# Performance work log

Measured on AMD Instinct MI355X. Metric: run time of the kernel, lower is better.

Reference implementation:

```python
import jax, jax.numpy as jnp
import numpy as np

N = 50000      # nodes
E = 800000     # edges
IN_DIM = 128
HID = 16       # per-head hidden dim (layer1)
HEADS = 8
OUT_DIM = 32   # layer2 output dim (1 head)
NEG_SLOPE = 0.2  # GAT-paper LeakyReLU slope


def _gat_layer(x, W, a_src, a_dst, src, dst, num_nodes):
    """One multi-head GAT layer.
    x: [N, Fin]; W: [Fin, H*D]; a_src/a_dst: [H, D]; src/dst: [E].
    Returns [N, H, D].
    """
    H, D = a_src.shape
    z = (x @ W).reshape(num_nodes, H, D)            # [N, H, D]
    # edge attention logits: attn_fc([z_src || z_dst]) split into two dots
    e_s = jnp.einsum('nhd,hd->nh', z, a_src)        # [N, H]
    e_d = jnp.einsum('nhd,hd->nh', z, a_dst)        # [N, H]
    e = e_s[src] + e_d[dst]                          # [E, H]
    e = jnp.where(e >= 0, e, NEG_SLOPE * e)          # leaky_relu
    # softmax over incoming edges of each destination node
    m = jax.ops.segment_max(e, dst, num_segments=num_nodes)   # [N, H]
    ex = jnp.exp(e - m[dst])                                   # [E, H]
    s = jax.ops.segment_sum(ex, dst, num_segments=num_nodes)  # [N, H]
    alpha = ex / s[dst]                                        # [E, H]
    msg = alpha[:, :, None] * z[src]                            # [E, H, D]
    return jax.ops.segment_sum(msg, dst, num_segments=num_nodes)  # [N, H, D]


def setup_inputs() -> dict:
    key = jax.random.key(0)
    ks = jax.random.split(key, 9)
    h = jax.random.normal(ks[0], (N, IN_DIM), dtype=jnp.float32)
    src = jax.random.randint(ks[1], (E,), 0, N, dtype=jnp.int32)
    dst = jax.random.randint(ks[2], (E,), 0, N, dtype=jnp.int32)
    sc1 = 1.0 / np.sqrt(IN_DIM)
    W1 = jax.random.normal(ks[3], (IN_DIM, HEADS * HID), dtype=jnp.float32) * sc1
    a1_src = jax.random.normal(ks[4], (HEADS, HID), dtype=jnp.float32) * 0.1
    a1_dst = jax.random.normal(ks[5], (HEADS, HID), dtype=jnp.float32) * 0.1
    sc2 = 1.0 / np.sqrt(HEADS * HID)
    W2 = jax.random.normal(ks[6], (HEADS * HID, OUT_DIM), dtype=jnp.float32) * sc2
    a2_src = jax.random.normal(ks[7], (1, OUT_DIM), dtype=jnp.float32) * 0.1
    a2_dst = jax.random.normal(ks[8], (1, OUT_DIM), dtype=jnp.float32) * 0.1
    return {"h": h, "W1": W1, "a1_src": a1_src, "a1_dst": a1_dst,
            "W2": W2, "a2_src": a2_src, "a2_dst": a2_dst,
            "src": src, "dst": dst}


def reference(h, W1, a1_src, a1_dst, W2, a2_src, a2_dst, src, dst):
    # layer1: multi-head, concat heads -> [N, HEADS*HID]
    h1 = _gat_layer(h, W1, a1_src, a1_dst, src, dst, N).reshape(N, HEADS * HID)
    h1 = jax.nn.elu(h1)
    # layer2: single head -> [N, OUT_DIM]
    out = _gat_layer(h1, W2, a2_src, a2_dst, src, dst, N).reshape(N, OUT_DIM)
    return out
```

## Files before the change

kernel.cpp:

```cpp
#include <hip/hip_runtime.h>
#include <hip/hip_fp16.h>
#include <math.h>

#define NN 50000
#define EE 800000
#define FIN 128
#define F1  128
#define NH  8
#define DH  16
#define F2  32
#define SLOPE 0.2f
#define LOG2E 1.44269504f

#define EB 4096
#define NBLK ((EE + EB - 1) / EB)
#define HB 2048
#define NHBLK ((EE + HB - 1) / HB)
#define BK  391
#define SEGCAP 4096
#define PREPB 80
#define GEMM1B ((NN + 63) / 64)
#define ATT1B  (((NN + 63) / 64) * 8)
#define GEMM2B ((NN + 63) / 64)

typedef _Float16 f16x8 __attribute__((ext_vector_type(8)));
typedef float    f32x4 __attribute__((ext_vector_type(4)));

__global__ __launch_bounds__(256) void k1_hist_prep(const int* __restrict__ dst,
        const float* __restrict__ W1, const float* __restrict__ W2,
        __half* __restrict__ wt1, __half* __restrict__ wt2, int* __restrict__ hist) {
    int tid = threadIdx.x;
    if (blockIdx.x < NHBLK) {
        __shared__ int lc[BK];
        for (int i = tid; i < BK; i += 256) lc[i] = 0;
        __syncthreads();
        int base = blockIdx.x * HB;
        int end = base + HB; if (end > EE) end = EE;
        for (int i = base + tid; i < end; i += 256)
            atomicAdd(&lc[dst[i] >> 7], 1);
        __syncthreads();
        for (int i = tid; i < BK; i += 256)
            if (lc[i]) atomicAdd(&hist[i], lc[i]);
    } else {
        int gidx = (blockIdx.x - NHBLK) * 256 + tid;
        if (gidx < FIN * F1) {
            int n = gidx >> 7, k = gidx & 127;
            wt1[gidx] = __float2half(W1[k * F1 + n]);
        } else {
            int t2 = gidx - FIN * F1;
            if (t2 < F2 * FIN) {
                int n = t2 >> 7, k = t2 & 127;
                wt2[t2] = __float2half(W2[k * F2 + n]);
            }
        }
    }
}

extern __shared__ char smem_k2[];
__global__ __launch_bounds__(256) void k2_split_gemm1(const int* __restrict__ src,
        const int* __restrict__ dst, const int* __restrict__ hist, int* __restrict__ cursor,
        unsigned int* __restrict__ sorted,
        const float* __restrict__ h, const __half* __restrict__ wt1,
        const float* __restrict__ a1s, const float* __restrict__ a1d,
        __half* __restrict__ z1s, float* __restrict__ es1x, float* __restrict__ ed1x) {
    int tid = threadIdx.x;
    if (blockIdx.x < NBLK) {
        unsigned int*   recs = (unsigned int*)smem_k2;
        unsigned short* rbk  = (unsigned short*)(smem_k2 + 16384);
        int* lc    = (int*)(smem_k2 + 24576);
        int* lofs  = (int*)(smem_k2 + 26624);
        int* lcur  = (int*)(smem_k2 + 28672);
        int* delta = (int*)(smem_k2 + 30720);
        int* bscan = (int*)(smem_k2 + 32768);
        int* sh    = (int*)(smem_k2 + 34816);
        for (int i = tid; i < 512; i += 256) lc[i] = 0;
        __syncthreads();
        int base = blockIdx.x * EB;
        int cnt = EE - base; if (cnt > EB) cnt = EB;
        unsigned int myrec[16];
        #pragma unroll
        for (int k = 0; k < 16; ++k) {
            int i = base + tid + k * 256;
            myrec[k] = 0xFFFFFFFFu;
            if (i - base < cnt) {
                unsigned int d = (unsigned int)dst[i];
                myrec[k] = (d << 16) | (unsigned int)src[i];
                atomicAdd(&lc[d >> 7], 1);
            }
        }
        __syncthreads();
        int a0 = lc[2 * tid], a1 = lc[2 * tid + 1];
        int tsum = a0 + a1;
        sh[tid] = tsum;
        __syncthreads();
        for (int off = 1; off < 256; off <<= 1) {
            int t = (tid >= off) ? sh[tid - off] : 0;
            __syncthreads(); sh[tid] += t; __syncthreads();
        }
        int ex = sh[tid] - tsum;
        lofs[2 * tid] = ex;
        lofs[2 * tid + 1] = ex + a0;
        __syncthreads();
        int h0 = hist[2 * tid], h1 = hist[2 * tid + 1];
        int hsum = h0 + h1;
        sh[tid] = hsum;
        __syncthreads();
        for (int off = 1; off < 256; off <<= 1) {
            int t = (tid >= off) ? sh[tid - off] : 0;
            __syncthreads(); sh[tid] += t; __syncthreads();
        }
        int hex = sh[tid] - hsum;
        bscan[2 * tid] = hex;
        bscan[2 * tid + 1] = hex + h0;
        __syncthreads();
        for (int b = tid; b < BK; b += 256) {
            int c = lc[b];
            lcur[b] = lofs[b];
            if (c) {
                int g = atomicAdd(&cursor[b], c);
                delta[b] = bscan[b] + g - lofs[b];
            }
        }
        __syncthreads();
        #pragma unroll
        for (int k = 0; k < 16; ++k) {
            if (myrec[k] != 0xFFFFFFFFu) {
                int b = (int)(myrec[k] >> 23);
                int pos = atomicAdd(&lcur[b], 1);
                recs[pos] = myrec[k];
                rbk[pos] = (unsigned short)b;
            }
        }
        __syncthreads();
        for (int s = tid; s < cnt; s += 256)
            sorted[s + delta[rbk[s]]] = recs[s];
    } else {
        __half* hs  = (__half*)smem_k2;
        __half* wls = (__half*)(smem_k2 + 17408);
        for (int c = tid; c < 2048; c += 256) {
            int row = c >> 4, ch = c & 15;
            *(float4*)&wls[row * 136 + ch * 8] = *(const float4*)&wt1[row * 128 + ch * 8];
        }
        int rowBase = (blockIdx.x - NBLK) * 64;
        for (int idx4 = tid; idx4 < 64 * 32; idx4 += 256) {
            int r = idx4 >> 5, cc = (idx4 & 31) * 4;
            int n = rowBase + r;
            float4 v = (n < NN) ? *(const float4*)&h[(size_t)n * FIN + cc] : make_float4(0, 0, 0, 0);
            union { __half2 h2[2]; int2 i; } u;
            u.h2[0] = __floats2half2_rn(v.x, v.y);
            u.h2[1] = __floats2half2_rn(v.z, v.w);
            *(int2*)&hs[r * 136 + cc] = u.i;
        }
        __syncthreads();
        int l = tid & 63, w = tid >> 6;
        int q = l >> 4, cl = l & 15;
        int m0 = w * 16;
        float as[8], ad[8];
        #pragma unroll
        for (int t = 0; t < 8; ++t) { as[t] = a1s[t * DH + cl]; ad[t] = a1d[t * DH + cl]; }
        f32x4 acc[8];
        #pragma unroll
        for (int t = 0; t < 8; ++t) acc[t] = (f32x4){0.f, 0.f, 0.f, 0.f};
        const __half* ap = &hs[(m0 + cl) * 136 + q * 8];
        const __half* bp = &wls[cl * 136 + q * 8];
        #pragma unroll
        for (int k0 = 0; k0 < 128; k0 += 32) {
            f16x8 af = *(const f16x8*)(ap + k0);
            #pragma unroll
            for (int t = 0; t < 8; ++t) {
                f16x8 bf = *(const f16x8*)(bp + t * 16 * 136 + k0);
                acc[t] = __builtin_amdgcn_mfma_f32_16x16x32_f16(af, bf, acc[t], 0, 0, 0);
            }
        }
        #pragma unroll
        for (int t = 0; t < 8; ++t) {
            #pragma unroll
            for (int reg = 0; reg < 4; ++reg) {
                int row = rowBase + m0 + q * 4 + reg;
                float z = acc[t][reg];
                float s = z * as[t], d = z * ad[t];
                s += __shfl_xor(s, 1, 64); d += __shfl_xor(d, 1, 64);
                s += __shfl_xor(s, 2, 64); d += __shfl_xor(d, 2, 64);
                s += __shfl_xor(s, 4, 64); d += __shfl_xor(d, 4, 64);
                s += __shfl_xor(s, 8, 64); d += __shfl_xor(d, 8, 64);
                if (row < NN) {
                    z1s[(size_t)t * (NN * 16) + (size_t)row * 16 + cl] = __float2half(z);
                    if (cl == 0) {
                        es1x[row * NH + t] = s * LOG2E;
                        ed1x[row * NH + t] = d * LOG2E;
                    }
                }
            }
        }
    }
}

__global__ __launch_bounds__(256) void csrbuild_kernel(const int* __restrict__ hist,
        const unsigned int* __restrict__ sorted, unsigned short* __restrict__ csr,
        const float* __restrict__ es1x, const float* __restrict__ ed1x,
        float* __restrict__ w1p, int* __restrict__ row_ptr) {
    __shared__ unsigned int recs[SEGCAP];
    __shared__ unsigned short csr_sh[SEGCAP];
    __shared__ unsigned char dst_sh[SEGCAP];
    __shared__ float ed_sh[128 * NH];
    __shared__ int ncnt[128], ncur[128];
    __shared__ int sh[256];
    __shared__ int bscan[512];
    int b = blockIdx.x;
    int tid = threadIdx.x;
    int h0 = hist[2 * tid], h1 = hist[2 * tid + 1];
    int hsum = h0 + h1;
    sh[tid] = hsum;
    if (tid < 128) ncnt[tid] = 0;
    for (int idx = tid; idx < 128 * NH; idx += 256) {
        int node = b * 128 + (idx >> 3);
        ed_sh[idx] = (node < NN) ? ed1x[node * NH + (idx & 7)] : 0.f;
    }
    __syncthreads();
    for (int off = 1; off < 256; off <<= 1) {
        int t = (tid >= off) ? sh[tid - off] : 0;
        __syncthreads(); sh[tid] += t; __syncthreads();
    }
    int hex = sh[tid] - hsum;
    bscan[2 * tid] = hex;
    bscan[2 * tid + 1] = hex + h0;
    __syncthreads();
    int s0 = bscan[b], s1 = bscan[b + 1];
    int cnt = s1 - s0; if (cnt > SEGCAP) cnt = SEGCAP;
    for (int i = tid; i < cnt; i += 256) {
        unsigned int r = sorted[s0 + i];
        recs[i] = r;
        atomicAdd(&ncnt[(r >> 16) & 127], 1);
    }
    __syncthreads();
    int v = (tid < 128) ? ncnt[tid] : 0;
    sh[tid] = v;
    __syncthreads();
    for (int off = 1; off < 256; off <<= 1) {
        int t = (tid >= off) ? sh[tid - off] : 0;
        __syncthreads(); sh[tid] += t; __syncthreads();
    }
    int ex = sh[tid] - v;
    if (tid < 128) {
        ncur[tid] = ex;
        int node = b * 128 + tid;
        if (node < NN) row_ptr[node] = s0 + ex;
    }
    if (b == BK - 1 && tid == 0) row_ptr[NN] = EE;
    __syncthreads();
    for (int i = tid; i < cnt; i += 256) {
        unsigned int r = recs[i];
        int local = (r >> 16) & 127;
        int p = atomicAdd(&ncur[local], 1);
        csr_sh[p] = (unsigned short)(r & 0xFFFFu);
        dst_sh[p] = (unsigned char)local;
    }
    __syncthreads();
    for (int i = tid; i < cnt; i += 256) {
        unsigned short sv = csr_sh[i];
        unsigned char lv = dst_sh[i];
        csr[s0 + i] = sv;
        float4 ea = *(const float4*)&es1x[(size_t)sv * NH];
        float4 eb = *(const float4*)&es1x[(size_t)sv * NH + 4];
        float es8[8] = {ea.x, ea.y, ea.z, ea.w, eb.x, eb.y, eb.z, eb.w};
        const float* edp = &ed_sh[(int)lv * NH];
        #pragma unroll
        for (int hh = 0; hh < 8; ++hh) {
            float e = es8[hh] + edp[hh];
            e = e >= 0.f ? e : SLOPE * e;
            w1p[(size_t)hh * EE + s0 + i] = exp2f(e);
        }
    }
}

__global__ __launch_bounds__(128, 8) void attn1_slice_kernel(const int* __restrict__ row_ptr,
        const unsigned short* __restrict__ csr, const __half* __restrict__ z1s,
        const float* __restrict__ w1p, __half* __restrict__ h1s) {
    int hl = blockIdx.x & 7;
    int n = (blockIdx.x >> 3) * 64 + (threadIdx.x >> 1);
    if (n >= NN) return;
    int j = threadIdx.x & 1;
    const __half* zp = z1s + (size_t)hl * (NN * 16) + j * 8;
    const float* wp = w1p + (size_t)hl * EE;
    int b0 = row_ptr[n];
    int cnt = row_ptr[n + 1] - b0;
    float acc[8] = {0.f, 0.f, 0.f, 0.f, 0.f, 0.f, 0.f, 0.f};
    float ws = 0.f;
    int i = 0;
    int pre = (4 - (b0 & 3)) & 3; if (pre > cnt) pre = cnt;
    for (; i < pre; ++i) {
        int s = csr[b0 + i];
        float wv = wp[b0 + i];
        ws += wv;
        union { float4 f; __half2 h2[4]; } u;
        u.f = *(const float4*)&zp[(size_t)s * 16];
        #pragma unroll
        for (int t = 0; t < 4; ++t) {
            float2 v = __half22float2(u.h2[t]);
            acc[2*t]   = fmaf(wv, v.x, acc[2*t]);
            acc[2*t+1] = fmaf(wv, v.y, acc[2*t+1]);
        }
    }
    int nb = (cnt - i) >> 2;
    if (nb > 0) {
        int e = b0 + i;
        ushort4 c4 = *(const ushort4*)&csr[e];
        float4  w4 = *(const float4*)&wp[e];
        for (int k = 1; k < nb; ++k) {
            ushort4 c4n = *(const ushort4*)&csr[e + 4];
            float4  w4n = *(const float4*)&wp[e + 4];
            union { float4 f; __half2 h2[4]; } u0, u1, u2, u3;
            u0.f = *(const float4*)&zp[(size_t)c4.x * 16];
            u1.f = *(const float4*)&zp[(size_t)c4.y * 16];
            u2.f = *(const float4*)&zp[(size_t)c4.z * 16];
            u3.f = *(const float4*)&zp[(size_t)c4.w * 16];
            ws += (w4.x + w4.y) + (w4.z + w4.w);
            #pragma unroll
            for (int t = 0; t < 4; ++t) {
                float2 v0 = __half22float2(u0.h2[t]);
                float2 v1 = __half22float2(u1.h2[t]);
                float2 v2 = __half22float2(u2.h2[t]);
                float2 v3 = __half22float2(u3.h2[t]);
                acc[2*t]   = fmaf(w4.x, v0.x, fmaf(w4.y, v1.x, fmaf(w4.z, v2.x, fmaf(w4.w, v3.x, acc[2*t]))));
                acc[2*t+1] = fmaf(w4.x, v0.y, fmaf(w4.y, v1.y, fmaf(w4.z, v2.y, fmaf(w4.w, v3.y, acc[2*t+1]))));
            }
            c4 = c4n; w4 = w4n; e += 4;
        }
        {
            union { float4 f; __half2 h2[4]; } u0, u1, u2, u3;
            u0.f = *(const float4*)&zp[(size_t)c4.x * 16];
            u1.f = *(const float4*)&zp[(size_t)c4.y * 16];
            u2.f = *(const float4*)&zp[(size_t)c4.z * 16];
            u3.f = *(const float4*)&zp[(size_t)c4.w * 16];
            ws += (w4.x + w4.y) + (w4.z + w4.w);
            #pragma unroll
            for (int t = 0; t < 4; ++t) {
                float2 v0 = __half22float2(u0.h2[t]);
                float2 v1 = __half22float2(u1.h2[t]);
                float2 v2 = __half22float2(u2.h2[t]);
                float2 v3 = __half22float2(u3.h2[t]);
                acc[2*t]   = fmaf(w4.x, v0.x, fmaf(w4.y, v1.x, fmaf(w4.z, v2.x, fmaf(w4.w, v3.x, acc[2*t]))));
                acc[2*t+1] = fmaf(w4.x, v0.y, fmaf(w4.y, v1.y, fmaf(w4.z, v2.y, fmaf(w4.w, v3.y, acc[2*t+1]))));
            }
        }
        i += nb << 2;
    }
    for (; i < cnt; ++i) {
        int s = csr[b0 + i];
        float wv = wp[b0 + i];
        ws += wv;
        union { float4 f; __half2 h2[4]; } u;
        u.f = *(const float4*)&zp[(size_t)s * 16];
        #pragma unroll
        for (int t = 0; t < 4; ++t) {
            float2 v = __half22float2(u.h2[t]);
            acc[2*t]   = fmaf(wv, v.x, acc[2*t]);
            acc[2*t+1] = fmaf(wv, v.y, acc[2*t+1]);
        }
    }
    float rs = ws > 0.f ? 1.0f / ws : 0.f;
    union { float4 f; __half2 h2[4]; } p;
    #pragma unroll
    for (int t = 0; t < 4; ++t) {
        float x0 = acc[2*t] * rs, x1 = acc[2*t+1] * rs;
        x0 = x0 > 0.f ? x0 : __expf(x0) - 1.0f;
        x1 = x1 > 0.f ? x1 : __expf(x1) - 1.0f;
        p.h2[t] = __floats2half2_rn(x0, x1);
    }
    *(float4*)&h1s[(size_t)hl * (NN * 16) + (size_t)n * 16 + j * 8] = p.f;
}

__global__ __launch_bounds__(256) void gemm2_kernel(const __half* __restrict__ h1s,
        const __half* __restrict__ wt2, const float* __restrict__ a2s, const float* __restrict__ a2d,
        __half* __restrict__ z2h, float* __restrict__ es2x, float* __restrict__ ed2x) {
    __shared__ alignas(16) __half hs[64 * 136];
    __shared__ alignas(16) __half wls[32 * 136];
    int tid = threadIdx.x;
    for (int c = tid; c < 512; c += 256) {
        int row = c >> 4, ch = c & 15;
        *(float4*)&wls[row * 136 + ch * 8] = *(const float4*)&wt2[row * 128 + ch * 8];
    }
    int rowBase = blockIdx.x * 64;
    for (int idx = tid; idx < 1024; idx += 256) {
        int j2 = idx & 1, nl = (idx >> 1) & 63, pl = idx >> 7;
        int n = rowBase + nl;
        float4 v = (n < NN) ? *(const float4*)&h1s[(size_t)pl * (NN * 16) + (size_t)n * 16 + j2 * 8]
                            : make_float4(0, 0, 0, 0);
        *(float4*)&hs[nl * 136 + pl * 16 + j2 * 8] = v;
    }
    __syncthreads();
    int l = tid & 63, w = tid >> 6;
    int q = l >> 4, cl = l & 15;
    int m0 = w * 16;
    float as0 = a2s[cl], as1 = a2s[16 + cl];
    float ad0 = a2d[cl], ad1 = a2d[16 + cl];
    f32x4 acc2[2];
    acc2[0] = (f32x4){0.f, 0.f, 0.f, 0.f};
    acc2[1] = (f32x4){0.f, 0.f, 0.f, 0.f};
    const __half* ap = &hs[(m0 + cl) * 136 + q * 8];
    const __half* bp = &wls[cl * 136 + q * 8];
    #pragma unroll
    for (int k0 = 0; k0 < 128; k0 += 32) {
        f16x8 af = *(const f16x8*)(ap + k0);
        #pragma unroll
        for (int t = 0; t < 2; ++t) {
            f16x8 bf = *(const f16x8*)(bp + t * 16 * 136 + k0);
            acc2[t] = __builtin_amdgcn_mfma_f32_16x16x32_f16(af, bf, acc2[t], 0, 0, 0);
        }
    }
    #pragma unroll
    for (int reg = 0; reg < 4; ++reg) {
        int row = rowBase + m0 + q * 4 + reg;
        float s = acc2[0][reg] * as0 + acc2[1][reg] * as1;
        float d = acc2[0][reg] * ad0 + acc2[1][reg] * ad1;
        s += __shfl_xor(s, 1, 64); d += __shfl_xor(d, 1, 64);
        s += __shfl_xor(s, 2, 64); d += __shfl_xor(d, 2, 64);
        s += __shfl_xor(s, 4, 64); d += __shfl_xor(d, 4, 64);
        s += __shfl_xor(s, 8, 64); d += __shfl_xor(d, 8, 64);
        if (row < NN) {
            z2h[(size_t)row * F2 + cl]      = __float2half(acc2[0][reg]);
            z2h[(size_t)row * F2 + 16 + cl] = __float2half(acc2[1][reg]);
            if (cl == 0) {
                es2x[row] = s * LOG2E;
                ed2x[row] = d * LOG2E;
            }
        }
    }
}

__global__ __launch_bounds__(128) void attn2_kernel(const int* __restrict__ row_ptr,
        const unsigned short* __restrict__ csr, const __half* __restrict__ z2h,
        const float* __restrict__ es, const float* __restrict__ ed,
        float* __restrict__ out) {
    int gt = blockIdx.x * 128 + threadIdx.x;
    int n = gt >> 3;
    int j = gt & 7;
    if (n >= NN) return;
    int b0 = row_ptr[n];
    int cnt = row_ptr[n + 1] - b0;
    float edn = ed[n];
    float acc[4] = {0.f, 0.f, 0.f, 0.f};
    float ws = 0.f;
    int i = 0;
    for (; i + 4 <= cnt; i += 4) {
        int s0 = csr[b0 + i], s1 = csr[b0 + i + 1], s2 = csr[b0 + i + 2], s3 = csr[b0 + i + 3];
        float e0 = es[s0] + edn;
        float e1 = es[s1] + edn;
        float e2 = es[s2] + edn;
        float e3 = es[s3] + edn;
        union { float2 f; __half2 h2[2]; } u0, u1, u2, u3;
        u0.f = *(const float2*)&z2h[(size_t)s0 * F2 + j * 4];
        u1.f = *(const float2*)&z2h[(size_t)s1 * F2 + j * 4];
        u2.f = *(const float2*)&z2h[(size_t)s2 * F2 + j * 4];
        u3.f = *(const float2*)&z2h[(size_t)s3 * F2 + j * 4];
        float w0 = exp2f(e0 >= 0.f ? e0 : SLOPE * e0);
        float w1 = exp2f(e1 >= 0.f ? e1 : SLOPE * e1);
        float w2 = exp2f(e2 >= 0.f ? e2 : SLOPE * e2);
        float w3 = exp2f(e3 >= 0.f ? e3 : SLOPE * e3);
        ws += (w0 + w1) + (w2 + w3);
        #pragma unroll
        for (int t = 0; t < 2; ++t) {
            float2 v0 = __half22float2(u0.h2[t]);
            float2 v1 = __half22float2(u1.h2[t]);
            float2 v2 = __half22float2(u2.h2[t]);
            float2 v3 = __half22float2(u3.h2[t]);
            acc[2*t]   = fmaf(w0, v0.x, fmaf(w1, v1.x, fmaf(w2, v2.x, fmaf(w3, v3.x, acc[2*t]))));
            acc[2*t+1] = fmaf(w0, v0.y, fmaf(w1, v1.y, fmaf(w2, v2.y, fmaf(w3, v3.y, acc[2*t+1]))));
        }
    }
    for (; i < cnt; ++i) {
        int s = csr[b0 + i];
        float e = es[s] + edn;
        float wv = exp2f(e >= 0.f ? e : SLOPE * e);
        ws += wv;
        union { float2 f; __half2 h2[2]; } u;
        u.f = *(const float2*)&z2h[(size_t)s * F2 + j * 4];
        #pragma unroll
        for (int t = 0; t < 2; ++t) {
            float2 v = __half22float2(u.h2[t]);
            acc[2*t]   = fmaf(wv, v.x, acc[2*t]);
            acc[2*t+1] = fmaf(wv, v.y, acc[2*t+1]);
        }
    }
    float rs = ws > 0.f ? 1.0f / ws : 0.f;
    *(float4*)&out[(size_t)n * F2 + j * 4] =
        make_float4(acc[0]*rs, acc[1]*rs, acc[2]*rs, acc[3]*rs);
}

extern "C" void kernel_launch(void* const* d_in, const int* in_sizes, int n_in,
                              void* d_out, int out_size, void* d_ws, size_t ws_size,
                              hipStream_t stream) {
    const float* h   = (const float*)d_in[0];
    const float* W1  = (const float*)d_in[1];
    const float* a1s = (const float*)d_in[2];
    const float* a1d = (const float*)d_in[3];
    const float* W2  = (const float*)d_in[4];
    const float* a2s = (const float*)d_in[5];
    const float* a2d = (const float*)d_in[6];
    const int*   src = (const int*)d_in[7];
    const int*   dst = (const int*)d_in[8];
    float* out = (float*)d_out;

    int* ip      = (int*)d_ws;
    int* hist    = ip;
    int* cursor  = hist + 512;
    int* row_ptr = cursor + 512;
    unsigned int* sorted = (unsigned int*)(row_ptr + NN + 8);
    unsigned short* csr16 = (unsigned short*)(sorted + EE);
    float* es1x = (float*)(csr16 + EE);
    float* ed1x = es1x + (size_t)NN * NH;
    float* es2x = ed1x + (size_t)NN * NH;
    float* ed2x = es2x + NN;
    __half* z1s = (__half*)(ed2x + NN);
    __half* z2h = z1s + (size_t)NN * F1;
    __half* wt1 = z2h + (size_t)NN * F2;
    __half* wt2 = wt1 + FIN * F1;
    __half* h1s = wt2 + F2 * FIN;
    float* w1p  = (float*)(h1s + (size_t)NN * F1);

    hipMemsetAsync(hist, 0, 1024 * sizeof(int), stream);

    k1_hist_prep<<<NHBLK + PREPB, 256, 0, stream>>>(dst, W1, W2, wt1, wt2, hist);
    k2_split_gemm1<<<NBLK + GEMM1B, 256, 52224, stream>>>(src, dst, hist, cursor, sorted,
                                                          h, wt1, a1s, a1d, z1s, es1x, ed1x);
    csrbuild_kernel<<<BK, 256, 0, stream>>>(hist, sorted, csr16, es1x, ed1x, w1p, row_ptr);
    attn1_slice_kernel<<<ATT1B, 128, 0, stream>>>(row_ptr, csr16, z1s, w1p, h1s);
    gemm2_kernel<<<GEMM2B, 256, 0, stream>>>(h1s, wt2, a2s, a2d, z2h, es2x, ed2x);
    attn2_kernel<<<(NN * 8 + 127) / 128, 128, 0, stream>>>(row_ptr, csr16, z2h, es2x, ed2x, out);
}
```

Measured before the change: 211.7 us.

## Stage per-tile CSR indices and edge weights in shared memory for layer-1 aggregation

The layer-1 attention aggregation now assigns 128 nodes per block (256 threads) and cooperatively loads each tile's contiguous CSR source indices and precomputed edge weights into shared memory in chunks, with coalesced global reads. Each thread pair then gathers z rows using indices and weights read from LDS instead of issuing per-thread strided global loads. This targets uncoalesced, latency-bound index and weight fetches. In exchange it adds block-wide barriers per chunk, which make threads wait on the highest-degree node in the tile, and uses more LDS per block, which may reduce occupancy.

```diff
diff --git a/kernel.cpp b/kernel.cpp
--- a/kernel.cpp
+++ b/kernel.cpp
@@ -20,8 +20,9 @@
 #define SEGCAP 4096
 #define PREPB 80
 #define GEMM1B ((NN + 63) / 64)
-#define ATT1B  (((NN + 63) / 64) * 8)
+#define ATT1B  (BK * 8)
 #define GEMM2B ((NN + 63) / 64)
+#define CHUNK 2560
 
 typedef _Float16 f16x8 __attribute__((ext_vector_type(8)));
 typedef float    f32x4 __attribute__((ext_vector_type(4)));
@@ -273,101 +274,84 @@
     }
 }
 
-__global__ __launch_bounds__(128, 8) void attn1_slice_kernel(const int* __restrict__ row_ptr,
+__global__ __launch_bounds__(256, 8) void attn1_slice_kernel(const int* __restrict__ row_ptr,
         const unsigned short* __restrict__ csr, const __half* __restrict__ z1s,
         const float* __restrict__ w1p, __half* __restrict__ h1s) {
+    __shared__ unsigned short csr_sh[CHUNK];
+    __shared__ float w_sh[CHUNK];
     int hl = blockIdx.x & 7;
-    int n = (blockIdx.x >> 3) * 64 + (threadIdx.x >> 1);
-    if (n >= NN) return;
-    int j = threadIdx.x & 1;
+    int tile = blockIdx.x >> 3;
+    int nodeBase = tile * 128;
+    int tid = threadIdx.x;
+    int n = nodeBase + (tid >> 1);
+    int j = tid & 1;
     const __half* zp = z1s + (size_t)hl * (NN * 16) + j * 8;
     const float* wp = w1p + (size_t)hl * EE;
-    int b0 = row_ptr[n];
-    int cnt = row_ptr[n + 1] - b0;
+    int tBeg = row_ptr[nodeBase];
+    int nEnd = nodeBase + 128; if (nEnd > NN) nEnd = NN;
+    int tEnd = row_ptr[nEnd];
+    int b0 = 0, b1 = -1;
+    if (n < NN) { b0 = row_ptr[n]; b1 = row_ptr[n + 1]; }
     float acc[8] = {0.f, 0.f, 0.f, 0.f, 0.f, 0.f, 0.f, 0.f};
     float ws = 0.f;
-    int i = 0;
-    int pre = (4 - (b0 & 3)) & 3; if (pre > cnt) pre = cnt;
-    for (; i < pre; ++i) {
-        int s = csr[b0 + i];
-        float wv = wp[b0 + i];
-        ws += wv;
-        union { float4 f; __half2 h2[4]; } u;
-        u.f = *(const float4*)&zp[(size_t)s * 16];
-        #pragma unroll
-        for (int t = 0; t < 4; ++t) {
-            float2 v = __half22float2(u.h2[t]);
-            acc[2*t]   = fmaf(wv, v.x, acc[2*t]);
-            acc[2*t+1] = fmaf(wv, v.y, acc[2*t+1]);
-        }
-    }
-    int nb = (cnt - i) >> 2;
-    if (nb > 0) {
-        int e = b0 + i;
-        ushort4 c4 = *(const ushort4*)&csr[e];
-        float4  w4 = *(const float4*)&wp[e];
-        for (int k = 1; k < nb; ++k) {
-            ushort4 c4n = *(const ushort4*)&csr[e + 4];
-            float4  w4n = *(const float4*)&wp[e + 4];
+    for (int c0 = tBeg; c0 < tEnd; c0 += CHUNK) {
+        int c1 = c0 + CHUNK; if (c1 > tEnd) c1 = tEnd;
+        for (int i = c0 + tid; i < c1; i += 256) {
+            csr_sh[i - c0] = csr[i];
+            w_sh[i - c0] = wp[i];
+        }
+        __syncthreads();
+        int lo = b0 > c0 ? b0 : c0;
+        int hi = b1 < c1 ? b1 : c1;
+        int i = lo;
+        for (; i + 4 <= hi; i += 4) {
+            int r = i - c0;
+            int s0 = csr_sh[r], s1 = csr_sh[r + 1], s2 = csr_sh[r + 2], s3 = csr_sh[r + 3];
+            float w0 = w_sh[r], w1 = w_sh[r + 1], w2 = w_sh[r + 2], w3 = w_sh[r + 3];
             union { float4 f; __half2 h2[4]; } u0, u1, u2, u3;
-            u0.f = *(const float4*)&zp[(size_t)c4.x * 16];
-            u1.f = *(const float4*)&zp[(size_t)c4.y * 16];
-            u2.f = *(const float4*)&zp[(size_t)c4.z * 16];
-            u3.f = *(const float4*)&zp[(size_t)c4.w * 16];
-            ws += (w4.x + w4.y) + (w4.z + w4.w);
+            u0.f = *(const float4*)&zp[(size_t)s0 * 16];
+            u1.f = *(const float4*)&zp[(size_t)s1 * 16];
+            u2.f = *(const float4*)&zp[(size_t)s2 * 16];
+            u3.f = *(const float4*)&zp[(size_t)s3 * 16];
+            ws += (w0 + w1) + (w2 + w3);
             #pragma unroll
             for (int t = 0; t < 4; ++t) {
                 float2 v0 = __half22float2(u0.h2[t]);
                 float2 v1 = __half22float2(u1.h2[t]);
                 float2 v2 = __half22float2(u2.h2[t]);
                 float2 v3 = __half22float2(u3.h2[t]);
-                acc[2*t]   = fmaf(w4.x, v0.x, fmaf(w4.y, v1.x, fmaf(w4.z, v2.x, fmaf(w4.w, v3.x, acc[2*t]))));
-                acc[2*t+1] = fmaf(w4.x, v0.y, fmaf(w4.y, v1.y, fmaf(w4.z, v2.y, fmaf(w4.w, v3.y, acc[2*t+1]))));
-            }
-            c4 = c4n; w4 = w4n; e += 4;
-        }
-        {
-            union { float4 f; __half2 h2[4]; } u0, u1, u2, u3;
-            u0.f = *(const float4*)&zp[(size_t)c4.x * 16];
-            u1.f = *(const float4*)&zp[(size_t)c4.y * 16];
-            u2.f = *(const float4*)&zp[(size_t)c4.z * 16];
-            u3.f = *(const float4*)&zp[(size_t)c4.w * 16];
-            ws += (w4.x + w4.y) + (w4.z + w4.w);
+                acc[2*t]   = fmaf(w0, v0.x, fmaf(w1, v1.x, fmaf(w2, v2.x, fmaf(w3, v3.x, acc[2*t]))));
+                acc[2*t+1] = fmaf(w0, v0.y, fmaf(w1, v1.y, fmaf(w2, v2.y, fmaf(w3, v3.y, acc[2*t+1]))));
+            }
+        }
+        for (; i < hi; ++i) {
+            int r = i - c0;
+            int s = csr_sh[r];
+            float wv = w_sh[r];
+            ws += wv;
+            union { float4 f; __half2 h2[4]; } u;
+            u.f = *(const float4*)&zp[(size_t)s * 16];
             #pragma unroll
             for (int t = 0; t < 4; ++t) {
-                float2 v0 = __half22float2(u0.h2[t]);
-                float2 v1 = __half22float2(u1.h2[t]);
-                float2 v2 = __half22float2(u2.h2[t]);
-                float2 v3 = __half22float2(u3.h2[t]);
-                acc[2*t]   = fmaf(w4.x, v0.x, fmaf(w4.y, v1.x, fmaf(w4.z, v2.x, fmaf(w4.w, v3.x, acc[2*t]))));
-                acc[2*t+1] = fmaf(w4.x, v0.y, fmaf(w4.y, v1.y, fmaf(w4.z, v2.y, fmaf(w4.w, v3.y, acc[2*t+1]))));
-            }
-        }
-        i += nb << 2;
-    }
-    for (; i < cnt; ++i) {
-        int s = csr[b0 + i];
-        float wv = wp[b0 + i];
-        ws += wv;
-        union { float4 f; __half2 h2[4]; } u;
-        u.f = *(const float4*)&zp[(size_t)s * 16];
+                float2 v = __half22float2(u.h2[t]);
+                acc[2*t]   = fmaf(wv, v.x, acc[2*t]);
+                acc[2*t+1] = fmaf(wv, v.y, acc[2*t+1]);
+            }
+        }
+        __syncthreads();
+    }
+    if (n < NN) {
+        float rs = ws > 0.f ? 1.0f / ws : 0.f;
+        union { float4 f; __half2 h2[4]; } p;
         #pragma unroll
         for (int t = 0; t < 4; ++t) {
-            float2 v = __half22float2(u.h2[t]);
-            acc[2*t]   = fmaf(wv, v.x, acc[2*t]);
-            acc[2*t+1] = fmaf(wv, v.y, acc[2*t+1]);
-        }
-    }
-    float rs = ws > 0.f ? 1.0f / ws : 0.f;
-    union { float4 f; __half2 h2[4]; } p;
-    #pragma unroll
-    for (int t = 0; t < 4; ++t) {
-        float x0 = acc[2*t] * rs, x1 = acc[2*t+1] * rs;
-        x0 = x0 > 0.f ? x0 : __expf(x0) - 1.0f;
-        x1 = x1 > 0.f ? x1 : __expf(x1) - 1.0f;
-        p.h2[t] = __floats2half2_rn(x0, x1);
-    }
-    *(float4*)&h1s[(size_t)hl * (NN * 16) + (size_t)n * 16 + j * 8] = p.f;
+            float x0 = acc[2*t] * rs, x1 = acc[2*t+1] * rs;
+            x0 = x0 > 0.f ? x0 : __expf(x0) - 1.0f;
+            x1 = x1 > 0.f ? x1 : __expf(x1) - 1.0f;
+            p.h2[t] = __floats2half2_rn(x0, x1);
+        }
+        *(float4*)&h1s[(size_t)hl * (NN * 16) + (size_t)n * 16 + j * 8] = p.f;
+    }
 }
 
 __global__ __launch_bounds__(256) void gemm2_kernel(const __half* __restrict__ h1s,
@@ -524,7 +508,7 @@
     k2_split_gemm1<<<NBLK + GEMM1B, 256, 52224, stream>>>(src, dst, hist, cursor, sorted,
                                                           h, wt1, a1s, a1d, z1s, es1x, ed1x);
     csrbuild_kernel<<<BK, 256, 0, stream>>>(hist, sorted, csr16, es1x, ed1x, w1p, row_ptr);
-    attn1_slice_kernel<<<ATT1B, 128, 0, stream>>>(row_ptr, csr16, z1s, w1p, h1s);
+    attn1_slice_kernel<<<ATT1B, 256, 0, stream>>>(row_ptr, csr16, z1s, w1p, h1s);
     gemm2_kernel<<<GEMM2B, 256, 0, stream>>>(h1s, wt2, a2s, a2d, z2h, es2x, ed2x);
     attn2_kernel<<<(NN * 8 + 127) / 128, 128, 0, stream>>>(row_ptr, csr16, z2h, es2x, ed2x, out);
 }
```

Result: faster. 200.6 us (-5.2%).
